# Optimization experiments

Hardware: AMD Instinct MI355X
Metric: run time of the kernel (lower is better)

The kernel has to match this reference:

```python
import jax, jax.numpy as jnp
import numpy as np

VOCAB, EMB = 30000, 300
HEADS, DPH = 8, 50
AD = HEADS * DPH            # att_dim_total = 400
MAX_LINES, MAX_WPL = 128, 32
BATCH = 16
NEG = 1e7                   # padding-mask penalty, matches torch source


def _split_heads(x):
    # [N, S, AD] -> [N, H, S, D]
    return x.reshape(x.shape[0], -1, HEADS, DPH).transpose(0, 2, 1, 3)


def _attention(q, k, v, mask_q=None, mask_k=None, mask_v=None):
    # Faithful port of MTHiSAN._attention. Note the (oddly named) torch masks:
    #   mask_q masks the KEY axis of scores, mask_k/mask_v zero the QUERY axis.
    scale = float(np.sqrt(q.shape[-1]))
    scores = jnp.einsum('bhqd,bhkd->bhqk', q, k) / scale
    if mask_q is not None:
        scores = scores - NEG * (~mask_q)[:, None, None, :].astype(scores.dtype)
    w = jax.nn.softmax(scores, axis=-1)
    if mask_k is not None:
        w = w * mask_k[:, None, :, None].astype(w.dtype)
    out = jnp.einsum('bhqk,bhkd->bhqd', w, v)
    if mask_v is not None:
        out = out * mask_v[:, None, :, None].astype(out.dtype)
    return out


def _forward(docs, emb, wq_w, wq_b, wk_w, wk_b, wv_w, wv_b, w_tgt,
             lq_w, lq_b, lk_w, lk_b, lv_w, lv_b, l_tgt,
             fc1_w, fc1_b, fc2_w, fc2_b):
    B = docs.shape[0]
    d = docs[:, :MAX_LINES * MAX_WPL].reshape(B * MAX_LINES, MAX_WPL)
    mask_w = d != 0                               # [B*L, W]
    mask_l = mask_w.sum(-1) != 0                  # [B*L]  non-empty lines
    # NOTE: instead of gathering non-empty lines (data-dependent shape), we keep
    # full shapes; masked word attention yields exact zeros for empty lines,
    # equivalent to the torch scatter into new_zeros.
    we = emb[d]                                   # [B*L, W, E] (dropout = eval/no-op)
    wq = jax.nn.elu(_split_heads(we @ wq_w + wq_b))
    wk = jax.nn.elu(_split_heads(we @ wk_w + wk_b))
    wv = jax.nn.elu(_split_heads(we @ wv_w + wv_b))
    watt = _attention(wq, wk, wv, mask_w, mask_w, mask_w)   # [B*L,H,W,D]
    # learned word-level target query (Linear(1, AD)(ones) == weight vector)
    tgt = jnp.broadcast_to(w_tgt.reshape(1, HEADS, 1, DPH),
                           (B * MAX_LINES, HEADS, 1, DPH))
    line_e = _attention(tgt, wk, watt, mask_q=mask_w)       # [B*L,H,1,D]
    line_e = line_e.transpose(0, 2, 1, 3).reshape(B * MAX_LINES, AD)
    line_e = line_e * mask_l[:, None].astype(line_e.dtype)  # zero empty lines
    line_e = line_e.reshape(B, MAX_LINES, AD)
    mask_l2 = mask_l.reshape(B, MAX_LINES)
    lq = jax.nn.elu(_split_heads(line_e @ lq_w + lq_b))
    lk = jax.nn.elu(_split_heads(line_e @ lk_w + lk_b))
    lv = jax.nn.elu(_split_heads(line_e @ lv_w + lv_b))
    latt = _attention(lq, lk, lv, mask_l2, mask_l2, mask_l2)  # [B,H,L,D]
    dtgt = jnp.broadcast_to(l_tgt.reshape(1, HEADS, 1, DPH), (B, HEADS, 1, DPH))
    doc_e = _attention(dtgt, lk, latt, mask_q=mask_l2)        # [B,H,1,D]
    doc_e = doc_e.transpose(0, 2, 1, 3).reshape(B, AD)
    logits1 = doc_e @ fc1_w + fc1_b   # task 'site'      [B,70]
    logits2 = doc_e @ fc2_w + fc2_b   # task 'histology' [B,512]
    return jnp.concatenate([logits1, logits2], axis=1)


def setup_inputs() -> dict:
    key = jax.random.key(0)
    ks = jax.random.split(key, 20)
    xavier = lambda k, i, o: (jax.random.normal(k, (i, o), jnp.float32)
                              * np.float32(np.sqrt(2.0 / (i + o))))
    emb = jax.random.normal(ks[0], (VOCAB, EMB), jnp.float32) * 0.02
    emb = emb.at[0].set(0.0)  # padding row zeroed as in __init__
    docs = jax.random.randint(ks[1], (BATCH, MAX_LINES * MAX_WPL), 0, VOCAB)
    z = lambda n: jnp.zeros((n,), jnp.float32)
    return dict(
        docs=docs, emb=emb,
        wq_w=xavier(ks[2], EMB, AD), wq_b=z(AD),
        wk_w=xavier(ks[3], EMB, AD), wk_b=z(AD),
        wv_w=xavier(ks[4], EMB, AD), wv_b=z(AD),
        w_tgt=jax.random.uniform(ks[5], (AD,), jnp.float32),
        lq_w=xavier(ks[6], AD, AD), lq_b=z(AD),
        lk_w=xavier(ks[7], AD, AD), lk_b=z(AD),
        lv_w=xavier(ks[8], AD, AD), lv_b=z(AD),
        l_tgt=jax.random.uniform(ks[9], (AD,), jnp.float32),
        fc1_w=xavier(ks[10], AD, 70), fc1_b=z(70),
        fc2_w=xavier(ks[11], AD, 512), fc2_b=z(512),
    )


def reference(docs, emb, wq_w, wq_b, wk_w, wk_b, wv_w, wv_b, w_tgt,
              lq_w, lq_b, lk_w, lk_b, lv_w, lv_b, l_tgt,
              fc1_w, fc1_b, fc2_w, fc2_b):
    return _forward(docs, emb, wq_w, wq_b, wk_w, wk_b, wv_w, wv_b, w_tgt,
                    lq_w, lq_b, lk_w, lk_b, lv_w, lv_b, l_tgt,
                    fc1_w, fc1_b, fc2_w, fc2_b)
```

## Files before the change

### kernel.cpp

```cpp
#include <hip/hip_runtime.h>
#include <math.h>

#define NLINES 2048
#define WPL 32
#define EMBD 300
#define AD 400
#define NH 8
#define DPH 50
#define QKV_S 52
#define SC_S 36
#define BATCH 16
#define LPD 128
#define NCOLS 1200
#define NPAD 1280
#define WLINE_FL 39936
#define HBLK 4992

typedef __bf16 bf16;
typedef bf16  v8bf  __attribute__((ext_vector_type(8)));
typedef float v4f   __attribute__((ext_vector_type(4)));
typedef float v16f  __attribute__((ext_vector_type(16)));

__device__ __forceinline__ float elu(float x) {
    return x > 0.f ? x : expm1f(x);
}
__device__ __forceinline__ float elu_fast(float x) {
    return x > 0.f ? x : (__expf(x) - 1.f);
}

#define SCALE 7.0710678118654755f

__device__ __forceinline__ void gld16(const bf16* g, bf16* l) {
    __builtin_amdgcn_global_load_lds(
        (const __attribute__((address_space(1))) void*)(g),
        (__attribute__((address_space(3))) void*)(l),
        16, 0, 0);
}

__global__ void split_rows(const float* __restrict__ src,
                           bf16* __restrict__ hi, bf16* __restrict__ lo,
                           int rows, int K, int K2)
{
    long idx = (long)blockIdx.x * 256 + threadIdx.x;
    if (idx >= (long)rows * K2) return;
    int r = (int)(idx / K2), k = (int)(idx - (long)r * K2);
    float x = (k < K) ? src[(long)r * K + k] : 0.f;
    bf16 h = (bf16)x;
    float hf = (float)h;
    bf16 l = (bf16)(x - hf);
    hi[idx] = h; lo[idx] = l;
}

__global__ void split_wt(const float* __restrict__ W0, const float* __restrict__ W1,
                         const float* __restrict__ W2,
                         const float* __restrict__ B0, const float* __restrict__ B1,
                         const float* __restrict__ B2,
                         bf16* __restrict__ hi, bf16* __restrict__ lo,
                         float* __restrict__ biasCat, int K, int K2)
{
    long idx = (long)blockIdx.x * 256 + threadIdx.x;
    if (idx >= (long)NPAD * K2) return;
    int n = (int)(idx / K2), k = (int)(idx - (long)n * K2);
    float x = 0.f;
    if (k < K && n < NCOLS) {
        int p = n / 400, c = n - p * 400;
        const float* W = (p == 0) ? W0 : (p == 1) ? W1 : W2;
        x = W[(long)k * 400 + c];
    }
    bf16 h = (bf16)x;
    float hf = (float)h;
    bf16 l = (bf16)(x - hf);
    hi[idx] = h; lo[idx] = l;
    if (k == 0) {
        float b = 0.f;
        if (n < NCOLS) {
            int p = n / 400, c = n - p * 400;
            const float* Bp = (p == 0) ? B0 : (p == 1) ? B1 : B2;
            b = Bp[c];
        }
        biasCat[n] = b;
    }
}

__launch_bounds__(256, 4)
__global__ void mfma_gemm(const bf16* __restrict__ Ah_t, const bf16* __restrict__ Al_t,
                          const int* __restrict__ docs,
                          const bf16* __restrict__ Bh_t, const bf16* __restrict__ Bl_t,
                          const float* __restrict__ biasCat,
                          float* __restrict__ C, int K2, int word_layout)
{
    __shared__ __align__(16) bf16 lds[2][4][2048];
    __shared__ int tok[128];

    const int tid = threadIdx.x;

    const int total = (int)(gridDim.x * gridDim.y);
    int flat = (int)(blockIdx.y * gridDim.x + blockIdx.x);
    if ((total & 7) == 0) flat = (flat & 7) * (total >> 3) + (flat >> 3);
    const int bx = flat % (int)gridDim.x;
    const int by = flat / (int)gridDim.x;
    const int row0 = by * 128;
    const int n0 = bx * 128;

    if (tid < 128) tok[tid] = docs ? docs[row0 + tid] : (row0 + tid);
    __syncthreads();

    const long abase = (long)tok[tid & 127] * K2 + (tid >> 7) * 8;
    const long bbase = (long)(n0 + (tid & 127)) * K2 + (tid >> 7) * 8;
    const int wb = (tid & ~63) * 8;

    const int wv = tid >> 6, lane = tid & 63;
    const int half = lane >> 5, r32 = lane & 31;
    const int wm0 = (wv >> 1) * 64, wn0 = (wv & 1) * 64;

    v16f acc[2][2];
    #pragma unroll
    for (int a = 0; a < 2; ++a)
        #pragma unroll
        for (int b = 0; b < 2; ++b) acc[a][b] = (v16f)0.f;

    auto STAGE = [&](int buf, int k0) {
        gld16(Ah_t + abase + k0, &lds[buf][0][wb]);
        gld16(Al_t + abase + k0, &lds[buf][1][wb]);
        gld16(Bh_t + bbase + k0, &lds[buf][2][wb]);
        gld16(Bl_t + bbase + k0, &lds[buf][3][wb]);
    };

    const int nk = K2 >> 4;
    STAGE(0, 0);
    __syncthreads();

    int cur = 0;
    for (int kt = 0; kt < nk; ++kt) {
        if (kt + 1 < nk) STAGE(cur ^ 1, (kt + 1) * 16);

        v8bf fa_h[2], fa_l[2], fb_h[2], fb_l[2];
        #pragma unroll
        for (int t = 0; t < 2; ++t) {
            const int ea = ((half << 7) + wm0 + t * 32 + r32) * 8;
            fa_h[t] = *(const v8bf*)&lds[cur][0][ea];
            fa_l[t] = *(const v8bf*)&lds[cur][1][ea];
            const int eb = ((half << 7) + wn0 + t * 32 + r32) * 8;
            fb_h[t] = *(const v8bf*)&lds[cur][2][eb];
            fb_l[t] = *(const v8bf*)&lds[cur][3][eb];
        }

        #pragma unroll
        for (int mt = 0; mt < 2; ++mt)
            #pragma unroll
            for (int nt = 0; nt < 2; ++nt)
                acc[mt][nt] = __builtin_amdgcn_mfma_f32_32x32x16_bf16(fa_h[mt], fb_h[nt], acc[mt][nt], 0, 0, 0);
        #pragma unroll
        for (int mt = 0; mt < 2; ++mt)
            #pragma unroll
            for (int nt = 0; nt < 2; ++nt)
                acc[mt][nt] = __builtin_amdgcn_mfma_f32_32x32x16_bf16(fa_h[mt], fb_l[nt], acc[mt][nt], 0, 0, 0);
        #pragma unroll
        for (int mt = 0; mt < 2; ++mt)
            #pragma unroll
            for (int nt = 0; nt < 2; ++nt)
                acc[mt][nt] = __builtin_amdgcn_mfma_f32_32x32x16_bf16(fa_l[mt], fb_h[nt], acc[mt][nt], 0, 0, 0);

        __syncthreads();
        cur ^= 1;
    }

    if (word_layout) {
        #pragma unroll
        for (int nt = 0; nt < 2; ++nt) {
            const int col = n0 + wn0 + nt * 32 + r32;
            if (col >= NCOLS) continue;
            const float bv = biasCat[col];
            const int p = col / 400;
            const int rem = col - p * 400;
            const int hh = rem / 50;
            const int d  = rem - hh * 50;
            #pragma unroll
            for (int mt = 0; mt < 2; ++mt) {
                const int rbase = row0 + wm0 + mt * 32 + 4 * half;
                #pragma unroll
                for (int rg = 0; rg < 16; ++rg) {
                    const int row = rbase + (rg & 3) + 8 * (rg >> 2);
                    const int ln = row >> 5, r = row & 31;
                    const long base = (((long)ln * NH + hh) * 3 + p) * 1664 + r * 52;
                    const float x = acc[mt][nt][rg] + bv;
                    C[base + d] = elu_fast(x);
                    if (d == 49) {
                        float2 z; z.x = 0.f; z.y = 0.f;
                        *(float2*)&C[base + 50] = z;
                    }
                }
            }
        }
    } else {
        #pragma unroll
        for (int nt = 0; nt < 2; ++nt) {
            const int col = n0 + wn0 + nt * 32 + r32;
            if (col >= NCOLS) continue;
            const float bv = biasCat[col];
            #pragma unroll
            for (int mt = 0; mt < 2; ++mt) {
                const int rbase = row0 + wm0 + mt * 32 + 4 * half;
                #pragma unroll
                for (int rg = 0; rg < 16; ++rg) {
                    const int row = rbase + (rg & 3) + 8 * (rg >> 2);
                    const float x = acc[mt][nt][rg] + bv;
                    C[(long)row * NCOLS + col] = elu_fast(x);
                }
            }
        }
    }
}

__launch_bounds__(256)
__global__ void word_attn4(const float* __restrict__ qkvw, const int* __restrict__ docs,
                           const float* __restrict__ w_tgt,
                           float* __restrict__ line_e, float* __restrict__ mask_l)
{
    __shared__ __align__(16) float sh[HBLK];
    __shared__ float sc[32 * 33];
    __shared__ float msk[WPL];
    __shared__ float tw[WPL];
    __shared__ float coefA[WPL];
    __shared__ float part[8][33];
    __shared__ float cw[WPL];
    __shared__ float vpart[4][64];
    __shared__ float tg[52];
    __shared__ float mls_s;

    const int tid = threadIdx.x;
    const int line = blockIdx.x >> 3;
    const int h = blockIdx.x & 7;

    if (tid < WPL) msk[tid] = (docs[line * WPL + tid] != 0) ? 1.f : 0.f;
    if (tid >= 64 && tid < 116) tg[tid - 64] = (tid - 64 < DPH) ? w_tgt[h * DPH + tid - 64] : 0.f;

    const float* src = qkvw + ((long)line * NH + h) * HBLK;
    for (int i = tid; i < HBLK / 4; i += 256)
        *(float4*)&sh[i * 4] = *(const float4*)&src[i * 4];
    __syncthreads();

    if (tid == 0) {
        float m = 0.f;
        for (int w = 0; w < WPL; ++w) m = fmaxf(m, msk[w]);
        mls_s = m;
        if (h == 0) mask_l[line] = m;
    }

    const int j = tid >> 3, kg = tid & 7;
    float4 qv[13];
    #pragma unroll
    for (int i = 0; i < 13; ++i) qv[i] = *(const float4*)&sh[j * 52 + i * 4];

    float e4[4];
    float m = -1e30f;
    #pragma unroll
    for (int c = 0; c < 4; ++c) {
        const int kk = kg * 4 + c;
        const float* kr = &sh[1664 + kk * 52];
        float s = 0.f;
        #pragma unroll
        for (int i = 0; i < 13; ++i) {
            const float4 kv = *(const float4*)&kr[i * 4];
            s += qv[i].x * kv.x + qv[i].y * kv.y + qv[i].z * kv.z + qv[i].w * kv.w;
        }
        s = s / SCALE - 1e7f * (1.f - msk[kk]);
        e4[c] = s;
        m = fmaxf(m, s);
    }
    m = fmaxf(m, __shfl_xor(m, 1));
    m = fmaxf(m, __shfl_xor(m, 2));
    m = fmaxf(m, __shfl_xor(m, 4));
    float rsum = 0.f;
    #pragma unroll
    for (int c = 0; c < 4; ++c) { e4[c] = __expf(e4[c] - m); rsum += e4[c]; }
    rsum += __shfl_xor(rsum, 1);
    rsum += __shfl_xor(rsum, 2);
    rsum += __shfl_xor(rsum, 4);
    #pragma unroll
    for (int c = 0; c < 4; ++c) sc[j * 33 + kg * 4 + c] = e4[c];

    if (tid < WPL) {
        const float* kr = &sh[1664 + tid * 52];
        float s = 0.f;
        #pragma unroll
        for (int i = 0; i < 25; ++i)
            s += tg[2 * i] * kr[2 * i] + tg[2 * i + 1] * kr[2 * i + 1];
        s = s / SCALE - 1e7f * (1.f - msk[tid]);
        float tm = s;
        #pragma unroll
        for (int off = 16; off >= 1; off >>= 1) tm = fmaxf(tm, __shfl_xor(tm, off, 32));
        const float te = __expf(s - tm);
        float tsum = te;
        #pragma unroll
        for (int off = 16; off >= 1; off >>= 1) tsum += __shfl_xor(tsum, off, 32);
        tw[tid] = te / tsum;
    }
    __syncthreads();

    if (kg == 0) coefA[j] = tw[j] * msk[j] / rsum;
    __syncthreads();

    {
        const int k = tid & 31, jg = tid >> 5;
        float cv = 0.f;
        #pragma unroll
        for (int t = 0; t < 4; ++t) {
            const int jj = jg * 4 + t;
            cv += coefA[jj] * sc[jj * 33 + k];
        }
        part[jg][k] = cv;
    }
    __syncthreads();
    if (tid < WPL) {
        float cv = 0.f;
        #pragma unroll
        for (int g = 0; g < 8; ++g) cv += part[g][tid];
        cw[tid] = cv;
    }
    __syncthreads();

    {
        const int d = tid & 63, kh = tid >> 6;
        float acc = 0.f;
        if (d < 52) {
            #pragma unroll
            for (int t = 0; t < 8; ++t) {
                const int k = kh * 8 + t;
                acc += cw[k] * sh[3328 + k * 52 + d];
            }
        }
        vpart[kh][d] = acc;
    }
    __syncthreads();
    if (tid < DPH) {
        const float o = vpart[0][tid] + vpart[1][tid] + vpart[2][tid] + vpart[3][tid];
        line_e[(long)line * AD + h * DPH + tid] = o * mls_s;
    }
}

__launch_bounds__(256)
__global__ void line_attn2(const float* __restrict__ Q, const float* __restrict__ Kp,
                           const float* __restrict__ Vp,
                           long DS, long HS, long LS,
                           const float* __restrict__ l_tgt, const float* __restrict__ mask_l,
                           float* __restrict__ doc_e)
{
    __shared__ float kl[LPD * 52];
    __shared__ float sc[64 * 130];
    __shared__ float ml[LPD];
    __shared__ float tw[LPD];
    __shared__ float cw[LPD];
    __shared__ float coefA[64];
    __shared__ float pm[4 * 64];
    __shared__ float ps[4 * 64];
    __shared__ float tg[52];
    __shared__ float rr[2];
    __shared__ float vpart[2][64];

    const int tid = threadIdx.x;
    const int doc = blockIdx.x >> 3;
    const int h = blockIdx.x & 7;
    const float* qbase = Q + doc * DS + h * HS;
    const float* kbase = Kp + doc * DS + h * HS;
    const float* vbase = Vp + doc * DS + h * HS;

    if (tid < LPD) { ml[tid] = mask_l[doc * LPD + tid]; cw[tid] = 0.f; }
    if (tid < 52) tg[tid] = (tid < DPH) ? l_tgt[h * DPH + tid] : 0.f;
    for (int idx = tid; idx < LPD * 52; idx += 256) {
        const int r = idx / 52, d = idx - r * 52;
        kl[idx] = (d < DPH) ? kbase[(long)r * LS + d] : 0.f;
    }
    __syncthreads();

    if (tid < LPD) {
        const float* kr = &kl[tid * 52];
        float s = 0.f;
        #pragma unroll
        for (int i = 0; i < 25; ++i)
            s += tg[2 * i] * kr[2 * i] + tg[2 * i + 1] * kr[2 * i + 1];
        tw[tid] = s / SCALE - 1e7f * (1.f - ml[tid]);
    }
    __syncthreads();
    if (tid < 64) {
        float a = fmaxf(tw[tid], tw[64 + tid]);
        #pragma unroll
        for (int off = 32; off >= 1; off >>= 1) a = fmaxf(a, __shfl_xor(a, off));
        if (tid == 0) rr[0] = a;
    }
    __syncthreads();
    if (tid < 64) {
        const float tm2 = rr[0];
        float a = __expf(tw[tid] - tm2) + __expf(tw[64 + tid] - tm2);
        #pragma unroll
        for (int off = 32; off >= 1; off >>= 1) a += __shfl_xor(a, off);
        if (tid == 0) rr[1] = a;
    }
    __syncthreads();
    if (tid < LPD) tw[tid] = __expf(tw[tid] - rr[0]) / rr[1];
    __syncthreads();

    const int j2 = tid & 63;
    const int kq = tid >> 6;

    for (int g = 0; g < 2; ++g) {
        const int j = g * 64 + j2;
        float2 qv[25];
        #pragma unroll
        for (int i = 0; i < 25; ++i)
            qv[i] = *(const float2*)(qbase + (long)j * LS + 2 * i);

        float m = -1e30f;
        for (int c = 0; c < 32; ++c) {
            const int k = kq * 32 + c;
            const float* kr = &kl[k * 52];
            float s = 0.f;
            #pragma unroll
            for (int i = 0; i < 25; ++i)
                s += qv[i].x * kr[2 * i] + qv[i].y * kr[2 * i + 1];
            s = s / SCALE - 1e7f * (1.f - ml[k]);
            sc[j2 * 130 + k] = s;
            m = fmaxf(m, s);
        }
        pm[kq * 64 + j2] = m;
        __syncthreads();
        const float rowm = fmaxf(fmaxf(pm[j2], pm[64 + j2]),
                                 fmaxf(pm[128 + j2], pm[192 + j2]));
        float sum = 0.f;
        for (int c = 0; c < 32; ++c) {
            const int k = kq * 32 + c;
            const float e = __expf(sc[j2 * 130 + k] - rowm);
            sc[j2 * 130 + k] = e;
            sum += e;
        }
        ps[kq * 64 + j2] = sum;
        __syncthreads();
        if (kq == 0) {
            const float rs = ps[j2] + ps[64 + j2] + ps[128 + j2] + ps[192 + j2];
            coefA[j2] = tw[j] * ml[j] / rs;
        }
        __syncthreads();
        if (tid < LPD) {
            float cv = 0.f;
            for (int jj = 0; jj < 64; ++jj)
                cv += coefA[jj] * sc[jj * 130 + tid];
            cw[tid] += cv;
        }
        __syncthreads();
    }

    const int d = tid & 63;
    const int half = (tid >> 6) & 1;
    if (tid < 128 && d < DPH) {
        float acc = 0.f;
        for (int k = half * 64; k < half * 64 + 64; ++k)
            acc += cw[k] * vbase[(long)k * LS + d];
        vpart[half][d] = acc;
    }
    __syncthreads();
    if (tid < DPH)
        doc_e[doc * AD + h * DPH + tid] = vpart[0][tid] + vpart[1][tid];
}

__launch_bounds__(256)
__global__ void word_attn(const float* __restrict__ qkv, const int* __restrict__ docs,
                          const float* __restrict__ w_tgt,
                          float* __restrict__ line_e, float* __restrict__ mask_l)
{
    __shared__ float qs[WPL * QKV_S];
    __shared__ float ks[WPL * QKV_S];
    __shared__ float vs[WPL * QKV_S];
    __shared__ float sc[WPL * SC_S];
    __shared__ float ts[WPL], tw[WPL], cw[WPL], msk[WPL];
    __shared__ float mls;

    const int tid = threadIdx.x;
    const int line = blockIdx.x;

    if (tid < WPL) msk[tid] = (docs[line * WPL + tid] != 0) ? 1.f : 0.f;
    __syncthreads();
    if (tid == 0) {
        float ml = 0.f;
        for (int w = 0; w < WPL; ++w) ml = fmaxf(ml, msk[w]);
        mls = ml;
        mask_l[line] = ml;
    }
    for (int h = 0; h < NH; ++h) {
        for (int idx = tid; idx < WPL * DPH; idx += 256) {
            const int r = idx / DPH, d = idx - r * DPH;
            const size_t base = (size_t)(line * WPL + r) * NCOLS + h * DPH + d;
            qs[r * QKV_S + d] = qkv[base];
            ks[r * QKV_S + d] = qkv[base + 400];
            vs[r * QKV_S + d] = qkv[base + 800];
        }
        __syncthreads();
        {
            const int j = tid >> 3, kg = tid & 7;
            #pragma unroll
            for (int c = 0; c < 4; ++c) {
                const int kk = kg * 4 + c;
                float s = 0.f;
                for (int dd = 0; dd < DPH; ++dd)
                    s += qs[j * QKV_S + dd] * ks[kk * QKV_S + dd];
                sc[j * SC_S + kk] = s / SCALE - 1e7f * (1.f - msk[kk]);
            }
        }
        if (tid < WPL) {
            float s = 0.f;
            for (int dd = 0; dd < DPH; ++dd)
                s += w_tgt[h * DPH + dd] * ks[tid * QKV_S + dd];
            ts[tid] = s / SCALE - 1e7f * (1.f - msk[tid]);
        }
        __syncthreads();
        if (tid < WPL) {
            const int j = tid;
            float m = -1e30f;
            for (int kk = 0; kk < WPL; ++kk) m = fmaxf(m, sc[j * SC_S + kk]);
            float sum = 0.f;
            for (int kk = 0; kk < WPL; ++kk) {
                const float e = expf(sc[j * SC_S + kk] - m);
                sc[j * SC_S + kk] = e;
                sum += e;
            }
            const float inv = 1.f / sum;
            for (int kk = 0; kk < WPL; ++kk) sc[j * SC_S + kk] *= inv;
        } else if (tid == WPL) {
            float m = -1e30f;
            for (int jj = 0; jj < WPL; ++jj) m = fmaxf(m, ts[jj]);
            float sum = 0.f;
            for (int jj = 0; jj < WPL; ++jj) { const float e = expf(ts[jj] - m); tw[jj] = e; sum += e; }
            const float inv = 1.f / sum;
            for (int jj = 0; jj < WPL; ++jj) tw[jj] *= inv;
        }
        __syncthreads();
        if (tid < WPL) {
            const int kk = tid;
            float c = 0.f;
            for (int jj = 0; jj < WPL; ++jj) c += tw[jj] * msk[jj] * sc[jj * SC_S + kk];
            cw[kk] = c;
        }
        __syncthreads();
        if (tid < DPH) {
            float acc = 0.f;
            for (int kk = 0; kk < WPL; ++kk) acc += cw[kk] * vs[kk * QKV_S + tid];
            line_e[line * AD + h * DPH + tid] = acc * mls;
        }
        __syncthreads();
    }
}

__launch_bounds__(256, 2)
__global__ void gemm_qkv(const float* __restrict__ Asrc,
                         const int* __restrict__ docs,
                         const float* __restrict__ emb,
                         const float* __restrict__ W0, const float* __restrict__ W1,
                         const float* __restrict__ W2,
                         const float* __restrict__ B0, const float* __restrict__ B1,
                         const float* __restrict__ B2,
                         float* __restrict__ C, int M, int K)
{
    __shared__ __align__(16) float As[32][132];
    __shared__ __align__(16) float Bs[32][132];

    const int tid = threadIdx.x;
    const int row0 = blockIdx.x * 128;
    const int n0 = blockIdx.y * 128;
    const int tc = tid & 15, tr = tid >> 4;

    float acc[2][2][4][4];
    #pragma unroll
    for (int a = 0; a < 2; ++a)
        #pragma unroll
        for (int b = 0; b < 2; ++b)
            #pragma unroll
            for (int c = 0; c < 4; ++c)
                #pragma unroll
                for (int d = 0; d < 4; ++d) acc[a][b][c][d] = 0.f;

    const int ma = tid & 127;
    const int kq = tid >> 7;
    const float* arow;
    if (docs) arow = emb + (size_t)docs[row0 + ma] * EMBD;
    else      arow = Asrc + (size_t)(row0 + ma) * K;

    const int gcol = n0 + ma;
    const int p = gcol / 400;
    const int ccol = gcol - p * 400;
    const float* Wp = (p == 0) ? W0 : (p == 1) ? W1 : W2;
    const bool colv = gcol < NCOLS;

    const int nk = (K + 31) >> 5;
    for (int ck = 0; ck < nk; ++ck) {
        const int k0 = ck * 32;
        #pragma unroll
        for (int f = 0; f < 4; ++f) {
            const int kl = kq * 16 + f * 4;
            const int kg = k0 + kl;
            float4 v = make_float4(0.f, 0.f, 0.f, 0.f);
            if (kg < K) v = *(const float4*)(arow + kg);
            As[kl + 0][ma] = v.x;
            As[kl + 1][ma] = v.y;
            As[kl + 2][ma] = v.z;
            As[kl + 3][ma] = v.w;
        }
        #pragma unroll
        for (int i = 0; i < 16; ++i) {
            const int kl = kq * 16 + i;
            const int kg = k0 + kl;
            float v = 0.f;
            if (colv && kg < K) v = Wp[(size_t)kg * 400 + ccol];
            Bs[kl][ma] = v;
        }
        __syncthreads();

        #pragma unroll 8
        for (int k = 0; k < 32; ++k) {
            const float4 a0 = *(const float4*)&As[k][tr * 4];
            const float4 a1 = *(const float4*)&As[k][64 + tr * 4];
            const float4 b0 = *(const float4*)&Bs[k][tc * 4];
            const float4 b1 = *(const float4*)&Bs[k][64 + tc * 4];
            const float ar[2][4] = {{a0.x, a0.y, a0.z, a0.w}, {a1.x, a1.y, a1.z, a1.w}};
            const float br[2][4] = {{b0.x, b0.y, b0.z, b0.w}, {b1.x, b1.y, b1.z, b1.w}};
            #pragma unroll
            for (int im = 0; im < 2; ++im)
                #pragma unroll
                for (int in_ = 0; in_ < 2; ++in_)
                    #pragma unroll
                    for (int rr = 0; rr < 4; ++rr)
                        #pragma unroll
                        for (int cc = 0; cc < 4; ++cc)
                            acc[im][in_][rr][cc] += ar[im][rr] * br[in_][cc];
        }
        __syncthreads();
    }

    #pragma unroll
    for (int in_ = 0; in_ < 2; ++in_) {
        const int ncol = n0 + in_ * 64 + tc * 4;
        if (ncol >= NCOLS) continue;
        const int pj = ncol / 400;
        const int cj = ncol - pj * 400;
        const float* Bp = (pj == 0) ? B0 : (pj == 1) ? B1 : B2;
        const float4 bv = *(const float4*)(Bp + cj);
        #pragma unroll
        for (int im = 0; im < 2; ++im) {
            #pragma unroll
            for (int rr = 0; rr < 4; ++rr) {
                const int row = row0 + im * 64 + tr * 4 + rr;
                float4 o;
                o.x = elu(acc[im][in_][rr][0] + bv.x);
                o.y = elu(acc[im][in_][rr][1] + bv.y);
                o.z = elu(acc[im][in_][rr][2] + bv.z);
                o.w = elu(acc[im][in_][rr][3] + bv.w);
                *(float4*)(C + (size_t)row * NCOLS + ncol) = o;
            }
        }
    }
}

__global__ void logits_kernel(const float* __restrict__ doc_e,
                              const float* __restrict__ fc1_w, const float* __restrict__ fc1_b,
                              const float* __restrict__ fc2_w, const float* __restrict__ fc2_b,
                              float* __restrict__ out)
{
    int o = blockIdx.x * blockDim.x + threadIdx.x;
    if (o >= BATCH * 582) return;
    int b = o / 582, jj = o - b * 582;
    const float* de = doc_e + b * AD;
    float acc;
    if (jj < 70) {
        acc = fc1_b[jj];
        for (int k = 0; k < AD; ++k) acc += de[k] * fc1_w[k * 70 + jj];
    } else {
        int j2 = jj - 70;
        acc = fc2_b[j2];
        for (int k = 0; k < AD; ++k) acc += de[k] * fc2_w[k * 512 + j2];
    }
    out[o] = acc;
}

extern "C" void kernel_launch(void* const* d_in, const int* in_sizes, int n_in,
                              void* d_out, int out_size, void* d_ws, size_t ws_size,
                              hipStream_t stream) {
    const int*   docs  = (const int*)  d_in[0];
    const float* emb   = (const float*)d_in[1];
    const float* wq_w  = (const float*)d_in[2];
    const float* wq_b  = (const float*)d_in[3];
    const float* wk_w  = (const float*)d_in[4];
    const float* wk_b  = (const float*)d_in[5];
    const float* wv_w  = (const float*)d_in[6];
    const float* wv_b  = (const float*)d_in[7];
    const float* w_tgt = (const float*)d_in[8];
    const float* lq_w  = (const float*)d_in[9];
    const float* lq_b  = (const float*)d_in[10];
    const float* lk_w  = (const float*)d_in[11];
    const float* lk_b  = (const float*)d_in[12];
    const float* lv_w  = (const float*)d_in[13];
    const float* lv_b  = (const float*)d_in[14];
    const float* l_tgt = (const float*)d_in[15];
    const float* fc1_w = (const float*)d_in[16];
    const float* fc1_b = (const float*)d_in[17];
    const float* fc2_w = (const float*)d_in[18];
    const float* fc2_b = (const float*)d_in[19];
    float* out = (float*)d_out;
    float* ws = (float*)d_ws;

    const long O_LINE_E = 0;
    const long O_MASK_L = 819200;
    const long O_DOC_E  = 821248;
    const long O_BIAS_W = 827648;
    const long O_BIAS_L = 828928;
    const long O_EMB_H  = 830208;
    const long O_EMB_L  = 5630208;
    const long O_WTW_H  = 10430208;
    const long O_WTW_L  = 10635008;
    const long O_WTL_H  = 10839808;
    const long O_WTL_L  = 11106048;
    const long O_LE_H   = 11372288;
    const long O_LE_L   = 11798272;
    const long O_R      = 12224256;

    const long LINE_QKV_FL = (long)NLINES * NCOLS;
    long ws_fl = (long)(ws_size / 4);
    long Rcap = ws_fl - O_R;

    if (Rcap >= LINE_QKV_FL) {
        float* line_e = ws + O_LINE_E;
        float* mask_l = ws + O_MASK_L;
        float* doc_e  = ws + O_DOC_E;
        float* bias_w = ws + O_BIAS_W;
        float* bias_l = ws + O_BIAS_L;
        bf16* embh = (bf16*)(ws + O_EMB_H);
        bf16* embl = (bf16*)(ws + O_EMB_L);
        bf16* wtwh = (bf16*)(ws + O_WTW_H);
        bf16* wtwl = (bf16*)(ws + O_WTW_L);
        bf16* wtlh = (bf16*)(ws + O_WTL_H);
        bf16* wtll = (bf16*)(ws + O_WTL_L);
        bf16* leh  = (bf16*)(ws + O_LE_H);
        bf16* lel  = (bf16*)(ws + O_LE_L);
        float* R   = ws + O_R;

        split_rows<<<(30000L * 320 + 255) / 256, 256, 0, stream>>>(emb, embh, embl, 30000, 300, 320);
        split_wt<<<((long)NPAD * 320 + 255) / 256, 256, 0, stream>>>(wq_w, wk_w, wv_w,
                                                                     wq_b, wk_b, wv_b,
                                                                     wtwh, wtwl, bias_w, 300, 320);
        split_wt<<<((long)NPAD * 416 + 255) / 256, 256, 0, stream>>>(lq_w, lk_w, lv_w,
                                                                     lq_b, lk_b, lv_b,
                                                                     wtlh, wtll, bias_l, 400, 416);

        long maxl = Rcap / WLINE_FL;
        if (maxl > 1024) maxl = 1024;
        long chunk = (maxl / 4) * 4;
        if (chunk < 4) chunk = 4;
        for (long c0 = 0; c0 < NLINES; c0 += chunk) {
            long cl = NLINES - c0 < chunk ? NLINES - c0 : chunk;
            dim3 g1(10, (unsigned)((cl * 32) / 128));
            mfma_gemm<<<g1, 256, 0, stream>>>(embh, embl, docs + c0 * WPL,
                                              wtwh, wtwl, bias_w, R, 320, 1);
            word_attn4<<<(unsigned)(cl * NH), 256, 0, stream>>>(R, docs + c0 * WPL, w_tgt,
                                                                line_e + c0 * AD, mask_l + c0);
        }

        split_rows<<<((long)NLINES * 416 + 255) / 256, 256, 0, stream>>>(line_e, leh, lel,
                                                                         NLINES, 400, 416);
        dim3 g2(10, NLINES / 128);
        mfma_gemm<<<g2, 256, 0, stream>>>(leh, lel, nullptr, wtlh, wtll, bias_l, R, 416, 0);
        line_attn2<<<BATCH * NH, 256, 0, stream>>>(R, R + 400, R + 800,
                                                   (long)LPD * NCOLS, (long)DPH, (long)NCOLS,
                                                   l_tgt, mask_l, doc_e);
        logits_kernel<<<(BATCH * 582 + 255) / 256, 256, 0, stream>>>(doc_e, fc1_w, fc1_b,
                                                                     fc2_w, fc2_b, out);
    } else {
        const long F_FIXED = 827648;
        const long PER_LINE_FL = (long)WPL * NCOLS;
        float* line_e = ws;
        float* mask_l = ws + 819200;
        float* doc_e  = ws + 821248;
        float* R      = ws + F_FIXED;
        long Rcap2 = ws_fl - F_FIXED;

        long maxl = Rcap2 / PER_LINE_FL;
        if (maxl > NLINES) maxl = NLINES;
        long maxl4 = (maxl / 4) * 4;
        int nc = (int)((NLINES + maxl4 - 1) / maxl4);
        int chunk = (int)((NLINES + nc - 1) / nc);
        chunk = ((chunk + 3) / 4) * 4;

        for (int c0 = 0; c0 < NLINES; c0 += chunk) {
            int cl = NLINES - c0 < chunk ? NLINES - c0 : chunk;
            dim3 g1((cl * 32) / 128, 10);
            gemm_qkv<<<g1, 256, 0, stream>>>(nullptr, docs + (size_t)c0 * WPL, emb,
                                             wq_w, wk_w, wv_w, wq_b, wk_b, wv_b,
                                             R, cl * 32, EMBD);
            word_attn<<<cl, 256, 0, stream>>>(R, docs + (size_t)c0 * WPL, w_tgt,
                                              line_e + (size_t)c0 * AD, mask_l + c0);
        }
        dim3 g2(16, 10);
        gemm_qkv<<<g2, 256, 0, stream>>>(line_e, nullptr, emb,
                                         lq_w, lk_w, lv_w, lq_b, lk_b, lv_b,
                                         R, NLINES, AD);
        line_attn2<<<BATCH * NH, 256, 0, stream>>>(R, R + 400, R + 800,
                                                   (long)LPD * NCOLS, (long)DPH, (long)NCOLS,
                                                   l_tgt, mask_l, doc_e);
        logits_kernel<<<(BATCH * 582 + 255) / 256, 256, 0, stream>>>(doc_e, fc1_w, fc1_b,
                                                                     fc2_w, fc2_b, out);
    }
}
```

Before: 680.0 us.

## Load B fragments directly from packed global layout, double K step per stage

The weight conversion kernel now writes the hi/lo bf16 split weights in a k-octet-major packed layout, so each lane can read its MFMA B fragment as one contiguous 16-byte global load. The B tiles no longer pass through LDS, and LDS now holds only the A tiles. Each stage covers 32 K values instead of 16, which halves the number of barriers and staging rounds. The cost is more global/L2 traffic for B, because each wave reloads the weights, and added load latency in the MFMA loop. Both K2 and the K/8 row count must also be compatible with the new packing.

```diff
diff --git a/kernel.cpp b/kernel.cpp
--- a/kernel.cpp
+++ b/kernel.cpp
@@ -70,7 +70,8 @@
     bf16 h = (bf16)x;
     float hf = (float)h;
     bf16 l = (bf16)(x - hf);
-    hi[idx] = h; lo[idx] = l;
+    const long pidx = ((long)(k >> 3) * NPAD + n) * 8 + (k & 7);
+    hi[pidx] = h; lo[pidx] = l;
     if (k == 0) {
         float b = 0.f;
         if (n < NCOLS) {
@@ -85,11 +86,11 @@
 __launch_bounds__(256, 4)
 __global__ void mfma_gemm(const bf16* __restrict__ Ah_t, const bf16* __restrict__ Al_t,
                           const int* __restrict__ docs,
-                          const bf16* __restrict__ Bh_t, const bf16* __restrict__ Bl_t,
+                          const bf16* __restrict__ Bh_p, const bf16* __restrict__ Bl_p,
                           const float* __restrict__ biasCat,
                           float* __restrict__ C, int K2, int word_layout)
 {
-    __shared__ __align__(16) bf16 lds[2][4][2048];
+    __shared__ __align__(16) bf16 lds[2][2][4096];
     __shared__ int tok[128];
 
     const int tid = threadIdx.x;
@@ -105,14 +106,17 @@
     if (tid < 128) tok[tid] = docs ? docs[row0 + tid] : (row0 + tid);
     __syncthreads();
 
-    const long abase = (long)tok[tid & 127] * K2 + (tid >> 7) * 8;
-    const long bbase = (long)(n0 + (tid & 127)) * K2 + (tid >> 7) * 8;
-    const int wb = (tid & ~63) * 8;
+    const int qa0 = tid >> 7;
+    const long abase = (long)tok[tid & 127] * K2;
+    const int wb = tid & ~63;
 
     const int wv = tid >> 6, lane = tid & 63;
     const int half = lane >> 5, r32 = lane & 31;
     const int wm0 = (wv >> 1) * 64, wn0 = (wv & 1) * 64;
 
+    const int colA = n0 + wn0 + r32;
+    const int colB = colA + 32;
+
     v16f acc[2][2];
     #pragma unroll
     for (int a = 0; a < 2; ++a)
@@ -120,49 +124,59 @@
         for (int b = 0; b < 2; ++b) acc[a][b] = (v16f)0.f;
 
     auto STAGE = [&](int buf, int k0) {
-        gld16(Ah_t + abase + k0, &lds[buf][0][wb]);
-        gld16(Al_t + abase + k0, &lds[buf][1][wb]);
-        gld16(Bh_t + bbase + k0, &lds[buf][2][wb]);
-        gld16(Bl_t + bbase + k0, &lds[buf][3][wb]);
+        const bf16* ga = Ah_t + abase + k0;
+        const bf16* gl = Al_t + abase + k0;
+        bf16* L0 = &lds[buf][0][wb * 8];
+        bf16* L1 = &lds[buf][1][wb * 8];
+        gld16(ga + qa0 * 8,       L0);
+        gld16(ga + (qa0 + 2) * 8, L0 + 2048);
+        gld16(gl + qa0 * 8,       L1);
+        gld16(gl + (qa0 + 2) * 8, L1 + 2048);
     };
 
-    const int nk = K2 >> 4;
+    const int nk = K2 >> 5;
     STAGE(0, 0);
     __syncthreads();
 
     int cur = 0;
     for (int kt = 0; kt < nk; ++kt) {
-        if (kt + 1 < nk) STAGE(cur ^ 1, (kt + 1) * 16);
-
-        v8bf fa_h[2], fa_l[2], fb_h[2], fb_l[2];
-        #pragma unroll
-        for (int t = 0; t < 2; ++t) {
-            const int ea = ((half << 7) + wm0 + t * 32 + r32) * 8;
-            fa_h[t] = *(const v8bf*)&lds[cur][0][ea];
-            fa_l[t] = *(const v8bf*)&lds[cur][1][ea];
-            const int eb = ((half << 7) + wn0 + t * 32 + r32) * 8;
-            fb_h[t] = *(const v8bf*)&lds[cur][2][eb];
-            fb_l[t] = *(const v8bf*)&lds[cur][3][eb];
-        }
-
-        #pragma unroll
-        for (int mt = 0; mt < 2; ++mt)
-            #pragma unroll
-            for (int nt = 0; nt < 2; ++nt)
-                acc[mt][nt] = __builtin_amdgcn_mfma_f32_32x32x16_bf16(fa_h[mt], fb_h[nt], acc[mt][nt], 0, 0, 0);
-        #pragma unroll
-        for (int mt = 0; mt < 2; ++mt)
-            #pragma unroll
-            for (int nt = 0; nt < 2; ++nt)
-                acc[mt][nt] = __builtin_amdgcn_mfma_f32_32x32x16_bf16(fa_h[mt], fb_l[nt], acc[mt][nt], 0, 0, 0);
-        #pragma unroll
-        for (int mt = 0; mt < 2; ++mt)
-            #pragma unroll
-            for (int nt = 0; nt < 2; ++nt)
-                acc[mt][nt] = __builtin_amdgcn_mfma_f32_32x32x16_bf16(fa_l[mt], fb_h[nt], acc[mt][nt], 0, 0, 0);
-
-        __syncthreads();
-        cur ^= 1;
+        if (kt + 1 < nk) STAGE(cur ^ 1, (kt + 1) * 32);
+
+        #pragma unroll
+        for (int ks = 0; ks < 2; ++ks) {
+            const long gb = (long)(kt * 4 + ks * 2 + half) * NPAD * 8;
+            v8bf fb_h[2], fb_l[2], fa_h[2], fa_l[2];
+            fb_h[0] = *(const v8bf*)&Bh_p[gb + (long)colA * 8];
+            fb_h[1] = *(const v8bf*)&Bh_p[gb + (long)colB * 8];
+            fb_l[0] = *(const v8bf*)&Bl_p[gb + (long)colA * 8];
+            fb_l[1] = *(const v8bf*)&Bl_p[gb + (long)colB * 8];
+            const int e0 = (((ks * 2 + half) << 7) + wm0 + r32) * 8;
+            fa_h[0] = *(const v8bf*)&lds[cur][0][e0];
+            fa_h[1] = *(const v8bf*)&lds[cur][0][e0 + 256];
+            fa_l[0] = *(const v8bf*)&lds[cur][1][e0];
+            fa_l[1] = *(const v8bf*)&lds[cur][1][e0 + 256];
+
+            #pragma unroll
+            for (int mt = 0; mt < 2; ++mt)
+                #pragma unroll
+                for (int nt = 0; nt < 2; ++nt)
+                    acc[mt][nt] = __builtin_amdgcn_mfma_f32_32x32x16_bf16(fa_h[mt], fb_h[nt], acc[mt][nt], 0, 0, 0);
+            #pragma unroll
+            for (int mt = 0; mt < 2; ++mt)
+                #pragma unroll
+                for (int nt = 0; nt < 2; ++nt)
+                    acc[mt][nt] = __builtin_amdgcn_mfma_f32_32x32x16_bf16(fa_h[mt], fb_l[nt], acc[mt][nt], 0, 0, 0);
+            #pragma unroll
+            for (int mt = 0; mt < 2; ++mt)
+                #pragma unroll
+                for (int nt = 0; nt < 2; ++nt)
+                    acc[mt][nt] = __builtin_amdgcn_mfma_f32_32x32x16_bf16(fa_l[mt], fb_h[nt], acc[mt][nt], 0, 0, 0);
+        }
+
+        if (kt + 1 < nk) {
+            __syncthreads();
+            cur ^= 1;
+        }
     }
 
     if (word_layout) {
```

Result: faster. 606.5 us (-10.8%).

## Interleave hi/lo bf16 operands and load GEMM fragments directly from global

Applied to the files above, without the earlier changes.

The bf16 hi/lo split buffers are merged into one packed layout. Each 8-element hi chunk sits next to its lo chunk, and the weights are stored k-major so lanes can read contiguous 16-byte fragments. The MFMA GEMM drops its double-buffered LDS staging (global_load_lds plus barriers) and reads A and B fragments straight from global memory into registers. The aim is to remove LDS traffic and per-step synchronisation. The cost is that cross-wave reuse through LDS is gone and software prefetch overlap is lost, so the kernel depends on cache hits and memory latency hiding.

```diff
diff --git a/kernel.cpp b/kernel.cpp
--- a/kernel.cpp
+++ b/kernel.cpp
@@ -30,16 +30,9 @@
 
 #define SCALE 7.0710678118654755f
 
-__device__ __forceinline__ void gld16(const bf16* g, bf16* l) {
-    __builtin_amdgcn_global_load_lds(
-        (const __attribute__((address_space(1))) void*)(g),
-        (__attribute__((address_space(3))) void*)(l),
-        16, 0, 0);
-}
-
-__global__ void split_rows(const float* __restrict__ src,
-                           bf16* __restrict__ hi, bf16* __restrict__ lo,
-                           int rows, int K, int K2)
+__global__ void split_rows_packed(const float* __restrict__ src,
+                                  bf16* __restrict__ pk,
+                                  int rows, int K, int K2)
 {
     long idx = (long)blockIdx.x * 256 + threadIdx.x;
     if (idx >= (long)rows * K2) return;
@@ -48,15 +41,16 @@
     bf16 h = (bf16)x;
     float hf = (float)h;
     bf16 l = (bf16)(x - hf);
-    hi[idx] = h; lo[idx] = l;
-}
-
-__global__ void split_wt(const float* __restrict__ W0, const float* __restrict__ W1,
-                         const float* __restrict__ W2,
-                         const float* __restrict__ B0, const float* __restrict__ B1,
-                         const float* __restrict__ B2,
-                         bf16* __restrict__ hi, bf16* __restrict__ lo,
-                         float* __restrict__ biasCat, int K, int K2)
+    const long p = ((long)r * (K2 >> 3) + (k >> 3)) * 16 + (k & 7);
+    pk[p] = h; pk[p + 8] = l;
+}
+
+__global__ void split_wt_packed(const float* __restrict__ W0, const float* __restrict__ W1,
+                                const float* __restrict__ W2,
+                                const float* __restrict__ B0, const float* __restrict__ B1,
+                                const float* __restrict__ B2,
+                                bf16* __restrict__ pk,
+                                float* __restrict__ biasCat, int K, int K2)
 {
     long idx = (long)blockIdx.x * 256 + threadIdx.x;
     if (idx >= (long)NPAD * K2) return;
@@ -70,7 +64,8 @@
     bf16 h = (bf16)x;
     float hf = (float)h;
     bf16 l = (bf16)(x - hf);
-    hi[idx] = h; lo[idx] = l;
+    const long pidx = ((long)(k >> 3) * NPAD + n) * 16 + (k & 7);
+    pk[pidx] = h; pk[pidx + 8] = l;
     if (k == 0) {
         float b = 0.f;
         if (n < NCOLS) {
@@ -83,13 +78,12 @@
 }
 
 __launch_bounds__(256, 4)
-__global__ void mfma_gemm(const bf16* __restrict__ Ah_t, const bf16* __restrict__ Al_t,
+__global__ void mfma_gemm(const bf16* __restrict__ Ap,
                           const int* __restrict__ docs,
-                          const bf16* __restrict__ Bh_t, const bf16* __restrict__ Bl_t,
+                          const bf16* __restrict__ Bp,
                           const float* __restrict__ biasCat,
                           float* __restrict__ C, int K2, int word_layout)
 {
-    __shared__ __align__(16) bf16 lds[2][4][2048];
     __shared__ int tok[128];
 
     const int tid = threadIdx.x;
@@ -105,64 +99,55 @@
     if (tid < 128) tok[tid] = docs ? docs[row0 + tid] : (row0 + tid);
     __syncthreads();
 
-    const long abase = (long)tok[tid & 127] * K2 + (tid >> 7) * 8;
-    const long bbase = (long)(n0 + (tid & 127)) * K2 + (tid >> 7) * 8;
-    const int wb = (tid & ~63) * 8;
-
     const int wv = tid >> 6, lane = tid & 63;
     const int half = lane >> 5, r32 = lane & 31;
     const int wm0 = (wv >> 1) * 64, wn0 = (wv & 1) * 64;
 
+    const int colA = n0 + wn0 + r32;
+    const int colB = colA + 32;
+
+    const long a0 = (long)tok[wm0 + r32]      * ((long)K2 * 2);
+    const long a1 = (long)tok[wm0 + 32 + r32] * ((long)K2 * 2);
+
     v16f acc[2][2];
     #pragma unroll
     for (int a = 0; a < 2; ++a)
         #pragma unroll
         for (int b = 0; b < 2; ++b) acc[a][b] = (v16f)0.f;
 
-    auto STAGE = [&](int buf, int k0) {
-        gld16(Ah_t + abase + k0, &lds[buf][0][wb]);
-        gld16(Al_t + abase + k0, &lds[buf][1][wb]);
-        gld16(Bh_t + bbase + k0, &lds[buf][2][wb]);
-        gld16(Bl_t + bbase + k0, &lds[buf][3][wb]);
-    };
-
-    const int nk = K2 >> 4;
-    STAGE(0, 0);
-    __syncthreads();
-
-    int cur = 0;
+    const int nk = K2 >> 5;
     for (int kt = 0; kt < nk; ++kt) {
-        if (kt + 1 < nk) STAGE(cur ^ 1, (kt + 1) * 16);
-
-        v8bf fa_h[2], fa_l[2], fb_h[2], fb_l[2];
-        #pragma unroll
-        for (int t = 0; t < 2; ++t) {
-            const int ea = ((half << 7) + wm0 + t * 32 + r32) * 8;
-            fa_h[t] = *(const v8bf*)&lds[cur][0][ea];
-            fa_l[t] = *(const v8bf*)&lds[cur][1][ea];
-            const int eb = ((half << 7) + wn0 + t * 32 + r32) * 8;
-            fb_h[t] = *(const v8bf*)&lds[cur][2][eb];
-            fb_l[t] = *(const v8bf*)&lds[cur][3][eb];
-        }
-
-        #pragma unroll
-        for (int mt = 0; mt < 2; ++mt)
-            #pragma unroll
-            for (int nt = 0; nt < 2; ++nt)
-                acc[mt][nt] = __builtin_amdgcn_mfma_f32_32x32x16_bf16(fa_h[mt], fb_h[nt], acc[mt][nt], 0, 0, 0);
-        #pragma unroll
-        for (int mt = 0; mt < 2; ++mt)
-            #pragma unroll
-            for (int nt = 0; nt < 2; ++nt)
-                acc[mt][nt] = __builtin_amdgcn_mfma_f32_32x32x16_bf16(fa_h[mt], fb_l[nt], acc[mt][nt], 0, 0, 0);
-        #pragma unroll
-        for (int mt = 0; mt < 2; ++mt)
-            #pragma unroll
-            for (int nt = 0; nt < 2; ++nt)
-                acc[mt][nt] = __builtin_amdgcn_mfma_f32_32x32x16_bf16(fa_l[mt], fb_h[nt], acc[mt][nt], 0, 0, 0);
-
-        __syncthreads();
-        cur ^= 1;
+        #pragma unroll
+        for (int ks = 0; ks < 2; ++ks) {
+            const int k0 = kt * 32 + (ks * 2 + half) * 8;
+            const bf16* bg = Bp + (long)(k0 >> 3) * NPAD * 16;
+            const long ka = (long)k0 * 2;
+            v8bf fb_h[2], fb_l[2], fa_h[2], fa_l[2];
+            fb_h[0] = *(const v8bf*)&bg[(long)colA * 16];
+            fb_l[0] = *(const v8bf*)&bg[(long)colA * 16 + 8];
+            fb_h[1] = *(const v8bf*)&bg[(long)colB * 16];
+            fb_l[1] = *(const v8bf*)&bg[(long)colB * 16 + 8];
+            fa_h[0] = *(const v8bf*)&Ap[a0 + ka];
+            fa_l[0] = *(const v8bf*)&Ap[a0 + ka + 8];
+            fa_h[1] = *(const v8bf*)&Ap[a1 + ka];
+            fa_l[1] = *(const v8bf*)&Ap[a1 + ka + 8];
+
+            #pragma unroll
+            for (int mt = 0; mt < 2; ++mt)
+                #pragma unroll
+                for (int nt = 0; nt < 2; ++nt)
+                    acc[mt][nt] = __builtin_amdgcn_mfma_f32_32x32x16_bf16(fa_h[mt], fb_h[nt], acc[mt][nt], 0, 0, 0);
+            #pragma unroll
+            for (int mt = 0; mt < 2; ++mt)
+                #pragma unroll
+                for (int nt = 0; nt < 2; ++nt)
+                    acc[mt][nt] = __builtin_amdgcn_mfma_f32_32x32x16_bf16(fa_h[mt], fb_l[nt], acc[mt][nt], 0, 0, 0);
+            #pragma unroll
+            for (int mt = 0; mt < 2; ++mt)
+                #pragma unroll
+                for (int nt = 0; nt < 2; ++nt)
+                    acc[mt][nt] = __builtin_amdgcn_mfma_f32_32x32x16_bf16(fa_l[mt], fb_h[nt], acc[mt][nt], 0, 0, 0);
+        }
     }
 
     if (word_layout) {
@@ -711,13 +696,9 @@
     const long O_BIAS_W = 827648;
     const long O_BIAS_L = 828928;
     const long O_EMB_H  = 830208;
-    const long O_EMB_L  = 5630208;
     const long O_WTW_H  = 10430208;
-    const long O_WTW_L  = 10635008;
     const long O_WTL_H  = 10839808;
-    const long O_WTL_L  = 11106048;
     const long O_LE_H   = 11372288;
-    const long O_LE_L   = 11798272;
     const long O_R      = 12224256;
 
     const long LINE_QKV_FL = (long)NLINES * NCOLS;
@@ -730,23 +711,19 @@
         float* doc_e  = ws + O_DOC_E;
         float* bias_w = ws + O_BIAS_W;
         float* bias_l = ws + O_BIAS_L;
-        bf16* embh = (bf16*)(ws + O_EMB_H);
-        bf16* embl = (bf16*)(ws + O_EMB_L);
-        bf16* wtwh = (bf16*)(ws + O_WTW_H);
-        bf16* wtwl = (bf16*)(ws + O_WTW_L);
-        bf16* wtlh = (bf16*)(ws + O_WTL_H);
-        bf16* wtll = (bf16*)(ws + O_WTL_L);
-        bf16* leh  = (bf16*)(ws + O_LE_H);
-        bf16* lel  = (bf16*)(ws + O_LE_L);
+        bf16* embp = (bf16*)(ws + O_EMB_H);
+        bf16* wtwp = (bf16*)(ws + O_WTW_H);
+        bf16* wtlp = (bf16*)(ws + O_WTL_H);
+        bf16* lep  = (bf16*)(ws + O_LE_H);
         float* R   = ws + O_R;
 
-        split_rows<<<(30000L * 320 + 255) / 256, 256, 0, stream>>>(emb, embh, embl, 30000, 300, 320);
-        split_wt<<<((long)NPAD * 320 + 255) / 256, 256, 0, stream>>>(wq_w, wk_w, wv_w,
-                                                                     wq_b, wk_b, wv_b,
-                                                                     wtwh, wtwl, bias_w, 300, 320);
-        split_wt<<<((long)NPAD * 416 + 255) / 256, 256, 0, stream>>>(lq_w, lk_w, lv_w,
-                                                                     lq_b, lk_b, lv_b,
-                                                                     wtlh, wtll, bias_l, 400, 416);
+        split_rows_packed<<<(30000L * 320 + 255) / 256, 256, 0, stream>>>(emb, embp, 30000, 300, 320);
+        split_wt_packed<<<((long)NPAD * 320 + 255) / 256, 256, 0, stream>>>(wq_w, wk_w, wv_w,
+                                                                            wq_b, wk_b, wv_b,
+                                                                            wtwp, bias_w, 300, 320);
+        split_wt_packed<<<((long)NPAD * 416 + 255) / 256, 256, 0, stream>>>(lq_w, lk_w, lv_w,
+                                                                            lq_b, lk_b, lv_b,
+                                                                            wtlp, bias_l, 400, 416);
 
         long maxl = Rcap / WLINE_FL;
         if (maxl > 1024) maxl = 1024;
@@ -755,16 +732,16 @@
         for (long c0 = 0; c0 < NLINES; c0 += chunk) {
             long cl = NLINES - c0 < chunk ? NLINES - c0 : chunk;
             dim3 g1(10, (unsigned)((cl * 32) / 128));
-            mfma_gemm<<<g1, 256, 0, stream>>>(embh, embl, docs + c0 * WPL,
-                                              wtwh, wtwl, bias_w, R, 320, 1);
+            mfma_gemm<<<g1, 256, 0, stream>>>(embp, docs + c0 * WPL,
+                                              wtwp, bias_w, R, 320, 1);
             word_attn4<<<(unsigned)(cl * NH), 256, 0, stream>>>(R, docs + c0 * WPL, w_tgt,
                                                                 line_e + c0 * AD, mask_l + c0);
         }
 
-        split_rows<<<((long)NLINES * 416 + 255) / 256, 256, 0, stream>>>(line_e, leh, lel,
-                                                                         NLINES, 400, 416);
+        split_rows_packed<<<((long)NLINES * 416 + 255) / 256, 256, 0, stream>>>(line_e, lep,
+                                                                                NLINES, 400, 416);
         dim3 g2(10, NLINES / 128);
-        mfma_gemm<<<g2, 256, 0, stream>>>(leh, lel, nullptr, wtlh, wtll, bias_l, R, 416, 0);
+        mfma_gemm<<<g2, 256, 0, stream>>>(lep, nullptr, wtlp, bias_l, R, 416, 0);
         line_attn2<<<BATCH * NH, 256, 0, stream>>>(R, R + 400, R + 800,
                                                    (long)LPD * NCOLS, (long)DPH, (long)NCOLS,
                                                    l_tgt, mask_l, doc_e);
```

Result: faster. 652.5 us (-4.0%).
